# Kernel tuning notes

Hardware: AMD Instinct MI355X
Metric: run time of the kernel (lower is better)

## Reference

```python
import jax, jax.numpy as jnp
import numpy as np

N = 50000       # nodes
E = 800000      # edges (before self loops)
F_IN = 256      # num_features
HID = 64        # hidden_dim
HEADS = 4       # num_heads
NEG = 0.2       # negative_slope
LN_EPS = 1e-5


def setup_inputs() -> dict:
    key = jax.random.key(0)
    ks = jax.random.split(key, 24)
    g = lambda k, shape, s=0.05: jax.random.normal(k, shape, jnp.float32) * s
    inp = {
        "x": jax.random.normal(ks[0], (N, F_IN), jnp.float32),
        "edge_index": jax.random.randint(ks[1], (2, E), 0, N, jnp.int32),
        # gat1: in=F_IN, out=HID per head, HEADS heads, concat=True
        "W1": g(ks[2], (HEADS * HID, F_IN)),
        "att_src1": g(ks[3], (HEADS, HID)),
        "att_dst1": g(ks[4], (HEADS, HID)),
        "b1": g(ks[5], (HEADS * HID,)),
        # gat2: in=HEADS*HID, out=HID, 1 head
        "W2": g(ks[6], (HID, HEADS * HID)),
        "att_src2": g(ks[7], (1, HID)),
        "att_dst2": g(ks[8], (1, HID)),
        "b2": g(ks[9], (HID,)),
        # lin_in residual projection
        "lin_w": g(ks[10], (HID, F_IN)),
        "lin_b": g(ks[11], (HID,)),
        # LayerNorm
        "gamma": jnp.ones((HID,), jnp.float32),
        "beta": jnp.zeros((HID,), jnp.float32),
        # GRU (1 layer, input=HID, hidden=HID), gate order r,z,n as in torch
        "w_ih": g(ks[12], (3 * HID, HID)),
        "w_hh": g(ks[13], (3 * HID, HID)),
        "b_ih": g(ks[14], (3 * HID,)),
        "b_hh": g(ks[15], (3 * HID,)),
        # fc head -> 3 classes
        "fc_w": g(ks[16], (3, HID)),
        "fc_b": g(ks[17], (3,)),
    }
    return inp


def gat_conv(x, W, att_src, att_dst, bias, src, dst, heads, n_nodes):
    """PyG-style GATConv (eval mode: no dropout). src/dst include self loops."""
    h = (x @ W.T).reshape(n_nodes, heads, -1)            # [N,H,C]
    a_src = jnp.einsum('nhc,hc->nh', h, att_src)          # [N,H]
    a_dst = jnp.einsum('nhc,hc->nh', h, att_dst)
    e = jax.nn.leaky_relu(a_src[src] + a_dst[dst], NEG)   # [E',H]
    m = jax.ops.segment_max(e, dst, num_segments=n_nodes) # scatter-softmax over dst
    e = jnp.exp(e - m[dst])
    s = jax.ops.segment_sum(e, dst, num_segments=n_nodes)
    alpha = e / s[dst]                                    # [E',H]
    out = jax.ops.segment_sum(alpha[:, :, None] * h[src], dst, num_segments=n_nodes)
    return out.reshape(n_nodes, -1) + bias                # concat heads + bias


def reference(x, edge_index, W1, att_src1, att_dst1, b1, W2, att_src2, att_dst2, b2,
              lin_w, lin_b, gamma, beta, w_ih, w_hh, b_ih, b_hh, fc_w, fc_b):
    n = x.shape[0]
    loops = jnp.arange(n, dtype=edge_index.dtype)
    src = jnp.concatenate([edge_index[0], loops])  # add_self_loops=True default
    dst = jnp.concatenate([edge_index[1], loops])

    h = jax.nn.leaky_relu(gat_conv(x, W1, att_src1, att_dst1, b1, src, dst, HEADS, n), NEG)
    # F.dropout is identity in eval mode
    h = gat_conv(h, W2, att_src2, att_dst2, b2, src, dst, 1, n)
    h = jax.nn.leaky_relu(h, NEG)
    # LayerNorm (torch uses biased variance)
    mu = h.mean(-1, keepdims=True)
    var = ((h - mu) ** 2).mean(-1, keepdims=True)
    h = (h - mu) / jnp.sqrt(var + LN_EPS) * gamma + beta
    h = h + x @ lin_w.T + lin_b
    # single-step GRU with h0 = 0 (seq_len == 1)
    gi = h @ w_ih.T + b_ih                 # [N,3C]
    i_r, i_z, i_n = jnp.split(gi, 3, axis=-1)
    h_r, h_z, h_n = jnp.split(b_hh, 3)     # W_hh @ 0 == 0
    r = jax.nn.sigmoid(i_r + h_r)
    z = jax.nn.sigmoid(i_z + h_z)
    ng = jnp.tanh(i_n + r * h_n)
    hy = (1.0 - z) * ng                    # + z * h_prev(=0)
    return hy @ fc_w.T + fc_b              # [N,3]
```

## Files before the change

kernel.cpp:

```cpp
#include <hip/hip_runtime.h>
#include <hip/hip_bf16.h>

#define N_NODES 50000
#define N_EDGES 800000
#define F_IN 256
#define HID 64
#define HEADS 4
#define NEG 0.2f
#define LN_EPS 1e-5f

typedef _Float16 half8 __attribute__((ext_vector_type(8)));
typedef _Float16 half4v __attribute__((ext_vector_type(4)));
typedef _Float16 half2v __attribute__((ext_vector_type(2)));
typedef float floatx4 __attribute__((ext_vector_type(4)));

union H2U { unsigned u; half2v h; };
union H8U { half8 v; half2v h2[4]; };

__device__ __forceinline__ float wave_sum(float v) {
    #pragma unroll
    for (int o = 32; o > 0; o >>= 1) v += __shfl_xor(v, o, 64);
    return v;
}
__device__ __forceinline__ float leaky(float x) { return x > 0.0f ? x : NEG * x; }

__global__ void bucket_scatter(const int* __restrict__ src, const int* __restrict__ dst,
                               int* __restrict__ deg, int* __restrict__ colb,
                               int E, int Etot) {
    int e = blockIdx.x * blockDim.x + threadIdx.x;
    if (e >= Etot) return;
    int s, d;
    if (e < E) { s = src[e]; d = dst[e]; }
    else       { s = d = e - E; }
    int pos = atomicAdd(&deg[d], 1);
    if (pos < 64) colb[d * 64 + pos] = s;
}

struct CvtJob { const float* src; _Float16* dst; int len; };
__global__ void cvt_f16_multi(CvtJob j0, CvtJob j1, CvtJob j2, CvtJob j3, CvtJob j4) {
    int idx = (blockIdx.x * blockDim.x + threadIdx.x) * 4;
    const float* s; _Float16* d; int rel = idx;
    if      (rel < j0.len) { s = j0.src; d = j0.dst; }
    else if ((rel -= j0.len) < j1.len) { s = j1.src; d = j1.dst; }
    else if ((rel -= j1.len) < j2.len) { s = j2.src; d = j2.dst; }
    else if ((rel -= j2.len) < j3.len) { s = j3.src; d = j3.dst; }
    else if ((rel -= j3.len) < j4.len) { s = j4.src; d = j4.dst; }
    else return;
    float4 v = *(const float4*)(s + rel);
    half4v h;
    h[0] = (_Float16)v.x; h[1] = (_Float16)v.y;
    h[2] = (_Float16)v.z; h[3] = (_Float16)v.w;
    *(half4v*)(d + rel) = h;
}

__device__ __forceinline__ half8 load_a8(const _Float16* p) { return *(const half8*)p; }
__device__ __forceinline__ half8 load_a8(const float* p) {
    float4 f0 = *(const float4*)p;
    float4 f1 = *(const float4*)(p + 4);
    half8 h;
    h[0] = (_Float16)f0.x; h[1] = (_Float16)f0.y;
    h[2] = (_Float16)f0.z; h[3] = (_Float16)f0.w;
    h[4] = (_Float16)f1.x; h[5] = (_Float16)f1.y;
    h[6] = (_Float16)f1.z; h[7] = (_Float16)f1.w;
    return h;
}

template<int NT, int H, typename OutT, typename AT>
__global__ __launch_bounds__(256, 2)
void gemm_mfma(const AT* __restrict__ A, const _Float16* __restrict__ B,
               const float* __restrict__ bias, OutT* __restrict__ Cout,
               const float* __restrict__ att_s, const float* __restrict__ att_d,
               float* __restrict__ a_srcO, float* __restrict__ a_dstO,
               int M, int K, int bias_mode) {
    constexpr int Nc = NT * 16;
    constexpr int BROW = 40;
    constexpr int BTILE = Nc * BROW * 2;
    constexpr int TILEB = 16 * Nc * sizeof(OutT);
    constexpr int SM = (BTILE > 4 * TILEB) ? BTILE : 4 * TILEB;
    __shared__ __align__(16) char smem[SM];
    _Float16* sB = (_Float16*)smem;
    int tid = threadIdx.x;
    int w = tid >> 6, lane = tid & 63;
    int m_base = blockIdx.x * 64 + w * 16;
    bool active = (m_base < M);
    int r = lane & 15, q = lane >> 4;
    const AT* ap = A + (size_t)(m_base + r) * K + q * 8;
    floatx4 acc[NT];
    #pragma unroll
    for (int t = 0; t < NT; ++t) acc[t] = (floatx4){0.f, 0.f, 0.f, 0.f};
    half8 a_next = {};
    if (active) a_next = load_a8(ap);
    for (int k0 = 0; k0 < K; k0 += 32) {
        for (int i = tid; i < Nc * 4; i += 256) {
            int row = i >> 2, seg = i & 3;
            *(half8*)(sB + row * BROW + seg * 8) =
                *(const half8*)(B + (size_t)row * K + k0 + seg * 8);
        }
        __syncthreads();
        half8 a = a_next;
        if (active && k0 + 32 < K) a_next = load_a8(ap + k0 + 32);
        if (active) {
            half8 b[NT];
            #pragma unroll
            for (int t = 0; t < NT; ++t)
                b[t] = *(const half8*)(sB + (t * 16 + r) * BROW + q * 8);
            #pragma unroll
            for (int t = 0; t < NT; ++t)
                acc[t] = __builtin_amdgcn_mfma_f32_16x16x32_f16(a, b[t], acc[t], 0, 0, 0);
        }
        __syncthreads();
    }
    if (active) {
        OutT* st = (OutT*)(smem + w * TILEB);
        #pragma unroll
        for (int t = 0; t < NT; ++t) {
            int cc = t * 16 + r;
            float bv = 0.f;
            if (bias_mode == 1) bv = bias[cc];
            else if (bias_mode == 2 && cc >= 256) bv = bias[cc - 256];
            #pragma unroll
            for (int rr = 0; rr < 4; ++rr)
                st[(q * 4 + rr) * Nc + cc] = (OutT)(acc[t][rr] + bv);
        }
        constexpr int NISS = TILEB / 1024;
        const int4* src = (const int4*)st;
        int4* dst = (int4*)((char*)Cout + (size_t)m_base * (Nc * sizeof(OutT)));
        #pragma unroll
        for (int i = 0; i < NISS; ++i) dst[i * 64 + lane] = src[i * 64 + lane];
        if constexpr (H > 0) {
            float ps[H][4], pd[H][4];
            #pragma unroll
            for (int h = 0; h < H; ++h) {
                #pragma unroll
                for (int rr = 0; rr < 4; ++rr) { ps[h][rr] = 0.f; pd[h][rr] = 0.f; }
                #pragma unroll
                for (int tt = 0; tt < 4; ++tt) {
                    int t = h * 4 + tt;
                    float as = att_s[t * 16 + r];
                    float ad = att_d[t * 16 + r];
                    #pragma unroll
                    for (int rr = 0; rr < 4; ++rr) {
                        ps[h][rr] += acc[t][rr] * as;
                        pd[h][rr] += acc[t][rr] * ad;
                    }
                }
            }
            #pragma unroll
            for (int m = 1; m < 16; m <<= 1) {
                #pragma unroll
                for (int h = 0; h < H; ++h)
                    #pragma unroll
                    for (int rr = 0; rr < 4; ++rr) {
                        ps[h][rr] += __shfl_xor(ps[h][rr], m, 64);
                        pd[h][rr] += __shfl_xor(pd[h][rr], m, 64);
                    }
            }
            if (r == 0) {
                #pragma unroll
                for (int rr = 0; rr < 4; ++rr) {
                    int gm = m_base + q * 4 + rr;
                    #pragma unroll
                    for (int h = 0; h < H; ++h) {
                        a_srcO[gm * H + h] = ps[h][rr];
                        a_dstO[gm * H + h] = pd[h][rr];
                    }
                }
            }
        }
    }
}

__global__ void gat_agg4(const _Float16* __restrict__ h, const float* __restrict__ a_src,
                         const float* __restrict__ a_dst, const int* __restrict__ degA,
                         const int* __restrict__ colb, const float* __restrict__ bias,
                         _Float16* __restrict__ outp, int N) {
    int w = threadIdx.x >> 6, lane = threadIdx.x & 63;
    int i = blockIdx.x * 4 + w;
    if (i >= N) return;
    __shared__ unsigned alphS[4][256];
    __shared__ int      scolS[4][64];
    unsigned* alph = alphS[w];
    int*      scol = scolS[w];
    int deg = degA[i];
    deg = deg > 64 ? 64 : deg;
    float4 ad4 = *(const float4*)(a_dst + i * 4);

    float e0 = 0.f, e1 = 0.f, e2 = 0.f, e3 = 0.f; int s = 0;
    if (lane < deg) {
        s = colb[i * 64 + lane];
        float4 as4 = *(const float4*)(a_src + (size_t)s * 4);
        e0 = __expf(leaky(as4.x + ad4.x));
        e1 = __expf(leaky(as4.y + ad4.y));
        e2 = __expf(leaky(as4.z + ad4.z));
        e3 = __expf(leaky(as4.w + ad4.w));
    }
    float s0 = wave_sum(e0), s1 = wave_sum(e1), s2 = wave_sum(e2), s3 = wave_sum(e3);
    float4 al = make_float4(0.f, 0.f, 0.f, 0.f);
    int so = 0;
    if (lane < deg) {
        al = make_float4(e0 / s0, e1 / s1, e2 / s2, e3 / s3);
        so = s * 640;
    }
    H2U p0, p1, p2, p3;
    _Float16 t0 = (_Float16)al.x; p0.h = (half2v){t0, t0};
    _Float16 t1 = (_Float16)al.y; p1.h = (half2v){t1, t1};
    _Float16 t2 = (_Float16)al.z; p2.h = (half2v){t2, t2};
    _Float16 t3 = (_Float16)al.w; p3.h = (half2v){t3, t3};
    *(uint4*)(alph + lane * 4) = make_uint4(p0.u, p1.u, p2.u, p3.u);
    scol[lane] = so;
    int half32 = lane >> 5;
    int fl = lane & 31;
    int flb = fl * 16;
    int ahofs = half32 * 4 + (fl >> 3);
    const char* hB = (const char*)h;
    float acc[8];
    #pragma unroll
    for (int k = 0; k < 8; ++k) acc[k] = 0.f;
    int dpad = (deg + 7) & ~7;
    for (int j = 0; j < dpad; j += 8) {
        int o0 = scol[j + half32];
        int o1 = scol[j + 2 + half32];
        int o2 = scol[j + 4 + half32];
        int o3 = scol[j + 6 + half32];
        H8U v0, v1, v2, v3;
        v0.v = *(const half8*)(hB + (flb + o0));
        v1.v = *(const half8*)(hB + (flb + o1));
        v2.v = *(const half8*)(hB + (flb + o2));
        v3.v = *(const half8*)(hB + (flb + o3));
        H2U a0, a1, a2, a3;
        a0.u = alph[j * 4 + ahofs];
        a1.u = alph[j * 4 + 8 + ahofs];
        a2.u = alph[j * 4 + 16 + ahofs];
        a3.u = alph[j * 4 + 24 + ahofs];
        #pragma unroll
        for (int p = 0; p < 4; ++p) {
            half2v hp = a0.h * v0.h2[p];
            hp = __builtin_elementwise_fma(a1.h, v1.h2[p], hp);
            hp = __builtin_elementwise_fma(a2.h, v2.h2[p], hp);
            hp = __builtin_elementwise_fma(a3.h, v3.h2[p], hp);
            acc[p * 2]     += (float)hp[0];
            acc[p * 2 + 1] += (float)hp[1];
        }
    }
    #pragma unroll
    for (int k = 0; k < 8; ++k) acc[k] += __shfl_xor(acc[k], 32, 64);
    if (lane < 32) {
        half8 o8;
        #pragma unroll
        for (int k = 0; k < 8; ++k)
            o8[k] = (_Float16)leaky(acc[k] + bias[fl * 8 + k]);
        *(half8*)(outp + (size_t)i * 256 + fl * 8) = o8;
    }
}

__global__ void gat_agg1_ln(const _Float16* __restrict__ h, const float* __restrict__ a_src,
                            const float* __restrict__ a_dst, const int* __restrict__ degA,
                            const int* __restrict__ colb, const float* __restrict__ bias,
                            const _Float16* __restrict__ linh, const float* __restrict__ gamma,
                            const float* __restrict__ beta, _Float16* __restrict__ hresh,
                            int N) {
    int w = threadIdx.x >> 6, lane = threadIdx.x & 63;
    int i = blockIdx.x * 4 + w;
    if (i >= N) return;
    __shared__ unsigned alphS[4][80];
    __shared__ int      scolS[4][80];
    unsigned* alph = alphS[w];
    int*      scol = scolS[w];
    int deg = degA[i];
    deg = deg > 64 ? 64 : deg;
    float ad = a_dst[i];
    int f0 = (lane & 7) * 8;
    float acc[8];
    #pragma unroll
    for (int k = 0; k < 8; ++k) acc[k] = 0.f;

    float e = 0.f; int s = 0;
    if (lane < deg) {
        s = colb[i * 64 + lane];
        e = __expf(leaky(a_src[s] + ad));
    }
    float ss = wave_sum(e);
    H2U pa; pa.u = 0;
    int so = 0;
    if (lane < deg) {
        _Float16 ah = (_Float16)(e / ss);
        pa.h = (half2v){ah, ah};
        so = s << 7;
    }
    alph[lane] = pa.u;
    scol[lane] = so;
    if (lane < 16) { alph[64 + lane] = 0; scol[64 + lane] = 0; }
    int g = lane >> 3;
    int fb = (lane & 7) * 16;
    const char* hB = (const char*)h;
    int dpad = (deg + 15) & ~15;
    for (int j = 0; j < dpad; j += 16) {
        int o0 = scol[j + g];
        int o1 = scol[j + 8 + g];
        H8U v0, v1;
        v0.v = *(const half8*)(hB + (fb + o0));
        v1.v = *(const half8*)(hB + (fb + o1));
        H2U a0, a1;
        a0.u = alph[j + g];
        a1.u = alph[j + 8 + g];
        #pragma unroll
        for (int p = 0; p < 4; ++p) {
            half2v hp = a0.h * v0.h2[p];
            hp = __builtin_elementwise_fma(a1.h, v1.h2[p], hp);
            acc[p * 2]     += (float)hp[0];
            acc[p * 2 + 1] += (float)hp[1];
        }
    }
    #pragma unroll
    for (int k = 0; k < 8; ++k) {
        acc[k] += __shfl_xor(acc[k], 8, 64);
        acc[k] += __shfl_xor(acc[k], 16, 64);
        acc[k] += __shfl_xor(acc[k], 32, 64);
    }
    float4 b0 = *(const float4*)(bias + f0);
    float4 b1 = *(const float4*)(bias + f0 + 4);
    float o[8];
    o[0] = leaky(acc[0] + b0.x); o[1] = leaky(acc[1] + b0.y);
    o[2] = leaky(acc[2] + b0.z); o[3] = leaky(acc[3] + b0.w);
    o[4] = leaky(acc[4] + b1.x); o[5] = leaky(acc[5] + b1.y);
    o[6] = leaky(acc[6] + b1.z); o[7] = leaky(acc[7] + b1.w);
    float ls = 0.f;
    #pragma unroll
    for (int k = 0; k < 8; ++k) ls += o[k];
    ls += __shfl_xor(ls, 1, 64); ls += __shfl_xor(ls, 2, 64); ls += __shfl_xor(ls, 4, 64);
    float mu = ls * (1.0f / 64.0f);
    float lq = 0.f;
    #pragma unroll
    for (int k = 0; k < 8; ++k) { o[k] -= mu; lq += o[k] * o[k]; }
    lq += __shfl_xor(lq, 1, 64); lq += __shfl_xor(lq, 2, 64); lq += __shfl_xor(lq, 4, 64);
    float rstd = rsqrtf(lq * (1.0f / 64.0f) + LN_EPS);
    float4 g0 = *(const float4*)(gamma + f0);
    float4 g1 = *(const float4*)(gamma + f0 + 4);
    float4 be0 = *(const float4*)(beta + f0);
    float4 be1 = *(const float4*)(beta + f0 + 4);
    half8 l8 = *(const half8*)(linh + (size_t)i * 320 + f0);
    if (lane < 8) {
        half8 hv;
        hv[0] = (_Float16)(o[0] * rstd * g0.x + be0.x + (float)l8[0]);
        hv[1] = (_Float16)(o[1] * rstd * g0.y + be0.y + (float)l8[1]);
        hv[2] = (_Float16)(o[2] * rstd * g0.z + be0.z + (float)l8[2]);
        hv[3] = (_Float16)(o[3] * rstd * g0.w + be0.w + (float)l8[3]);
        hv[4] = (_Float16)(o[4] * rstd * g1.x + be1.x + (float)l8[4]);
        hv[5] = (_Float16)(o[5] * rstd * g1.y + be1.y + (float)l8[5]);
        hv[6] = (_Float16)(o[6] * rstd * g1.z + be1.z + (float)l8[6]);
        hv[7] = (_Float16)(o[7] * rstd * g1.w + be1.w + (float)l8[7]);
        *(half8*)(hresh + (size_t)i * 64 + f0) = hv;
    }
}

__global__ __launch_bounds__(256, 2)
void gemm_gru(const _Float16* __restrict__ A, const _Float16* __restrict__ B,
              const float* __restrict__ b_ih, const float* __restrict__ b_hh,
              const float* __restrict__ fc_w, const float* __restrict__ fc_b,
              float* __restrict__ outp, int M) {
    const int K = 64, NT = 12, Nc = 192;
    constexpr int BROW = 40;
    __shared__ __align__(16) char smem[4 * 16 * 192 * 2];
    _Float16* sB = (_Float16*)smem;
    int tid = threadIdx.x;
    int w = tid >> 6, lane = tid & 63;
    int m_base = blockIdx.x * 64 + w * 16;
    bool active = (m_base < M);
    int r = lane & 15, q = lane >> 4;
    const _Float16* ap = A + (size_t)(m_base + r) * K + q * 8;
    floatx4 acc[NT];
    #pragma unroll
    for (int t = 0; t < NT; ++t) acc[t] = (floatx4){0.f, 0.f, 0.f, 0.f};
    half8 a_next = {};
    if (active) a_next = *(const half8*)ap;
    for (int k0 = 0; k0 < K; k0 += 32) {
        for (int i = tid; i < Nc * 4; i += 256) {
            int row = i >> 2, seg = i & 3;
            *(half8*)(sB + row * BROW + seg * 8) =
                *(const half8*)(B + (size_t)row * K + k0 + seg * 8);
        }
        __syncthreads();
        half8 a = a_next;
        if (active && k0 + 32 < K) a_next = *(const half8*)(ap + k0 + 32);
        if (active) {
            half8 b[NT];
            #pragma unroll
            for (int t = 0; t < NT; ++t)
                b[t] = *(const half8*)(sB + (t * 16 + r) * BROW + q * 8);
            #pragma unroll
            for (int t = 0; t < NT; ++t)
                acc[t] = __builtin_amdgcn_mfma_f32_16x16x32_f16(a, b[t], acc[t], 0, 0, 0);
        }
        __syncthreads();
    }
    if (!active) return;
    _Float16* sw = (_Float16*)smem + w * 16 * 192;
    #pragma unroll
    for (int t = 0; t < NT; ++t) {
        int cc = t * 16 + r;
        float bv = b_ih[cc];
        #pragma unroll
        for (int rr = 0; rr < 4; ++rr)
            sw[(q * 4 + rr) * Nc + cc] = (_Float16)(acc[t][rr] + bv);
    }
    float br_[4], bz_[4], bn_[4], f0_[4], f1_[4], f2_[4];
    *(float4*)br_ = *(const float4*)(b_hh + r * 4);
    *(float4*)bz_ = *(const float4*)(b_hh + 64 + r * 4);
    *(float4*)bn_ = *(const float4*)(b_hh + 128 + r * 4);
    *(float4*)f0_ = *(const float4*)(fc_w + r * 4);
    *(float4*)f1_ = *(const float4*)(fc_w + 64 + r * 4);
    *(float4*)f2_ = *(const float4*)(fc_w + 128 + r * 4);
    #pragma unroll
    for (int rr = 0; rr < 4; ++rr) {
        int row = q * 4 + rr;
        const _Float16* g = sw + row * Nc;
        half4v ir4 = *(const half4v*)(g + r * 4);
        half4v iz4 = *(const half4v*)(g + 64 + r * 4);
        half4v in4 = *(const half4v*)(g + 128 + r * 4);
        float p0 = 0.f, p1 = 0.f, p2 = 0.f;
        #pragma unroll
        for (int k = 0; k < 4; ++k) {
            float rg = 1.0f / (1.0f + __expf(-((float)ir4[k] + br_[k])));
            float zg = 1.0f / (1.0f + __expf(-((float)iz4[k] + bz_[k])));
            float ng = tanhf((float)in4[k] + rg * bn_[k]);
            float hy = (1.0f - zg) * ng;
            p0 += hy * f0_[k]; p1 += hy * f1_[k]; p2 += hy * f2_[k];
        }
        #pragma unroll
        for (int o = 1; o <= 8; o <<= 1) {
            p0 += __shfl_xor(p0, o, 64);
            p1 += __shfl_xor(p1, o, 64);
            p2 += __shfl_xor(p2, o, 64);
        }
        if (r == 0) {
            int gm = m_base + row;
            outp[(size_t)gm * 3 + 0] = p0 + fc_b[0];
            outp[(size_t)gm * 3 + 1] = p1 + fc_b[1];
            outp[(size_t)gm * 3 + 2] = p2 + fc_b[2];
        }
    }
}

extern "C" void kernel_launch(void* const* d_in, const int* in_sizes, int n_in,
                              void* d_out, int out_size, void* d_ws, size_t ws_size,
                              hipStream_t stream) {
    const float* x        = (const float*)d_in[0];
    const int*   ei       = (const int*)d_in[1];
    const float* W1       = (const float*)d_in[2];
    const float* att_src1 = (const float*)d_in[3];
    const float* att_dst1 = (const float*)d_in[4];
    const float* b1       = (const float*)d_in[5];
    const float* W2       = (const float*)d_in[6];
    const float* att_src2 = (const float*)d_in[7];
    const float* att_dst2 = (const float*)d_in[8];
    const float* b2       = (const float*)d_in[9];
    const float* lin_w    = (const float*)d_in[10];
    const float* lin_b    = (const float*)d_in[11];
    const float* gamma    = (const float*)d_in[12];
    const float* beta     = (const float*)d_in[13];
    const float* w_ih     = (const float*)d_in[14];
    const float* b_ih     = (const float*)d_in[16];
    const float* b_hh     = (const float*)d_in[17];
    const float* fc_w     = (const float*)d_in[18];
    const float* fc_b     = (const float*)d_in[19];
    float* out = (float*)d_out;

    const int N = N_NODES, E = N_EDGES;
    const int Etot = E + N;
    char* ws = (char*)d_ws;

    size_t off = 0;
    auto alloc = [&](size_t bytes) {
        size_t o = off;
        off = (off + bytes + 255) & ~(size_t)255;
        return o;
    };
    int*      deg     = (int*)(ws + alloc((size_t)N * 4));
    int*      colb    = (int*)(ws + alloc((size_t)N * 64 * 4));
    float*    a_src1b = (float*)(ws + alloc((size_t)N * HEADS * 4));
    float*    a_dst1b = (float*)(ws + alloc((size_t)N * HEADS * 4));
    float*    a_src2b = (float*)(ws + alloc((size_t)N * 4));
    float*    a_dst2b = (float*)(ws + alloc((size_t)N * 4));
    _Float16* B1big   = (_Float16*)(ws + alloc((size_t)320 * 256 * 2));
    _Float16* W1h     = B1big;
    _Float16* lin_wh  = B1big + 256 * 256;
    _Float16* W2h     = (_Float16*)(ws + alloc((size_t)64 * 256 * 2));
    _Float16* w_ihh   = (_Float16*)(ws + alloc((size_t)192 * 64 * 2));
    _Float16* h1L  = (_Float16*)(ws + alloc((size_t)32000000));
    char* r3 = ws + alloc((size_t)25600000);
    _Float16* o1h   = (_Float16*)r3;
    _Float16* hresh = (_Float16*)r3;
    char* r4 = ws + alloc((size_t)6400000);
    _Float16* h2h = (_Float16*)r4;

    hipMemsetAsync(deg, 0, (size_t)N * 4, stream);

    bucket_scatter<<<(Etot + 255) / 256, 256, 0, stream>>>(ei, ei + E, deg, colb, E, Etot);

    {
        CvtJob j0{W1, W1h, 256 * 256};
        CvtJob j1{W2, W2h, 64 * 256};
        CvtJob j2{lin_w, lin_wh, 64 * 256};
        CvtJob j3{w_ih, w_ihh, 192 * 64};
        CvtJob j4{nullptr, nullptr, 0};
        int total4 = (j0.len + j1.len + j2.len + j3.len) / 4;
        cvt_f16_multi<<<(total4 + 255) / 256, 256, 0, stream>>>(j0, j1, j2, j3, j4);
    }

    const int gmBlocks = (N + 63) / 64;
    const int aggBlocks = (N + 3) / 4;

    gemm_mfma<20, 4, _Float16, float><<<gmBlocks, 256, 0, stream>>>(x, B1big, lin_b, h1L,
        att_src1, att_dst1, a_src1b, a_dst1b, N, 256, 2);
    gat_agg4<<<aggBlocks, 256, 0, stream>>>(h1L, a_src1b, a_dst1b, deg, colb, b1, o1h, N);

    gemm_mfma<4, 1, _Float16, _Float16><<<gmBlocks, 256, 0, stream>>>(o1h, W2h, nullptr, h2h,
        att_src2, att_dst2, a_src2b, a_dst2b, N, 256, 0);

    gat_agg1_ln<<<aggBlocks, 256, 0, stream>>>(h2h, a_src2b, a_dst2b, deg, colb, b2,
        h1L + 256, gamma, beta, hresh, N);

    gemm_gru<<<gmBlocks, 256, 0, stream>>>(hresh, w_ihh, b_ih, b_hh, fc_w, fc_b, out, N);
}
```

Before: 322.8 us.

## Fuse W2 projection into layer-1 aggregation and GRU head into layer-2 aggregation

The W2 GEMM with its attention dot products moves into gat_agg4 as a per-wave fdot2 matvec over an LDS row, so the 256-wide o1 intermediate no longer round-trips through global memory. The GRU input GEMM and FC head move into gat_agg1_ln the same way, which removes the separate gemm_gru kernel and the hresh buffer. Edge bucketing and weight conversion merge into one prep kernel, and W2 and w_ih are pre-transposed into k-pair-major layouts for coalesced per-lane loads. The cost is that MFMA tensor-core GEMMs become scalar dot2 matvecs that reread weights per node, which could make the aggregation kernels compute- or cache-bound.

```diff
diff --git a/kernel.cpp b/kernel.cpp
--- a/kernel.cpp
+++ b/kernel.cpp
@@ -24,33 +24,60 @@
 }
 __device__ __forceinline__ float leaky(float x) { return x > 0.0f ? x : NEG * x; }
 
-__global__ void bucket_scatter(const int* __restrict__ src, const int* __restrict__ dst,
-                               int* __restrict__ deg, int* __restrict__ colb,
-                               int E, int Etot) {
-    int e = blockIdx.x * blockDim.x + threadIdx.x;
-    if (e >= Etot) return;
-    int s, d;
-    if (e < E) { s = src[e]; d = dst[e]; }
-    else       { s = d = e - E; }
-    int pos = atomicAdd(&deg[d], 1);
-    if (pos < 64) colb[d * 64 + pos] = s;
-}
-
-struct CvtJob { const float* src; _Float16* dst; int len; };
-__global__ void cvt_f16_multi(CvtJob j0, CvtJob j1, CvtJob j2, CvtJob j3, CvtJob j4) {
-    int idx = (blockIdx.x * blockDim.x + threadIdx.x) * 4;
-    const float* s; _Float16* d; int rel = idx;
-    if      (rel < j0.len) { s = j0.src; d = j0.dst; }
-    else if ((rel -= j0.len) < j1.len) { s = j1.src; d = j1.dst; }
-    else if ((rel -= j1.len) < j2.len) { s = j2.src; d = j2.dst; }
-    else if ((rel -= j2.len) < j3.len) { s = j3.src; d = j3.dst; }
-    else if ((rel -= j3.len) < j4.len) { s = j4.src; d = j4.dst; }
-    else return;
-    float4 v = *(const float4*)(s + rel);
-    half4v h;
-    h[0] = (_Float16)v.x; h[1] = (_Float16)v.y;
-    h[2] = (_Float16)v.z; h[3] = (_Float16)v.w;
-    *(half4v*)(d + rel) = h;
+__device__ __forceinline__ float dot2acc(half2v a, half2v b, float c) {
+#if __has_builtin(__builtin_amdgcn_fdot2)
+    return __builtin_amdgcn_fdot2(a, b, c, false);
+#else
+    half2v p = a * b;
+    return c + (float)p[0] + (float)p[1];
+#endif
+}
+
+__global__ void prep_kernel(const int* __restrict__ src, const int* __restrict__ dst,
+                            int* __restrict__ deg, int* __restrict__ colb,
+                            const float* __restrict__ W1, const float* __restrict__ lin_w,
+                            _Float16* __restrict__ B1big,
+                            const float* __restrict__ W2, _Float16* __restrict__ w2p,
+                            const float* __restrict__ w_ih, _Float16* __restrict__ wihp,
+                            int E, int Etot, int SB) {
+    if ((int)blockIdx.x < SB) {
+        int e = blockIdx.x * 256 + threadIdx.x;
+        if (e >= Etot) return;
+        int s, d;
+        if (e < E) { s = src[e]; d = dst[e]; }
+        else       { s = d = e - E; }
+        int pos = atomicAdd(&deg[d], 1);
+        if (pos < 64) colb[d * 64 + pos] = s;
+        return;
+    }
+    int t = (blockIdx.x - SB) * 256 + threadIdx.x;
+    if (t < 20480) {
+        int rel = t * 4;
+        const float* s; _Float16* d;
+        if (rel < 65536) { s = W1; d = B1big; }
+        else { rel -= 65536; s = lin_w; d = B1big + 65536; }
+        float4 v = *(const float4*)(s + rel);
+        half4v h;
+        h[0] = (_Float16)v.x; h[1] = (_Float16)v.y;
+        h[2] = (_Float16)v.z; h[3] = (_Float16)v.w;
+        *(half4v*)(d + rel) = h;
+    } else {
+        int t2 = t - 20480;
+        if (t2 < 8192) {
+            int c = t2 & 63, k2 = t2 >> 6;
+            half2v h;
+            h[0] = (_Float16)W2[c * 256 + 2 * k2];
+            h[1] = (_Float16)W2[c * 256 + 2 * k2 + 1];
+            *(half2v*)(w2p + (k2 * 64 + c) * 2) = h;
+        } else if (t2 < 8192 + 6144) {
+            int t3 = t2 - 8192;
+            int c = t3 % 192, k2 = t3 / 192;
+            half2v h;
+            h[0] = (_Float16)w_ih[c * 64 + 2 * k2];
+            h[1] = (_Float16)w_ih[c * 64 + 2 * k2 + 1];
+            *(half2v*)(wihp + (k2 * 192 + c) * 2) = h;
+        }
+    }
 }
 
 __device__ __forceinline__ half8 load_a8(const _Float16* p) { return *(const half8*)p; }
@@ -173,14 +200,19 @@
 __global__ void gat_agg4(const _Float16* __restrict__ h, const float* __restrict__ a_src,
                          const float* __restrict__ a_dst, const int* __restrict__ degA,
                          const int* __restrict__ colb, const float* __restrict__ bias,
-                         _Float16* __restrict__ outp, int N) {
+                         const _Float16* __restrict__ w2p,
+                         const float* __restrict__ att_s2, const float* __restrict__ att_d2,
+                         _Float16* __restrict__ h2h, float* __restrict__ a_src2,
+                         float* __restrict__ a_dst2, int N) {
     int w = threadIdx.x >> 6, lane = threadIdx.x & 63;
     int i = blockIdx.x * 4 + w;
     if (i >= N) return;
     __shared__ unsigned alphS[4][256];
     __shared__ int      scolS[4][64];
+    __shared__ __align__(16) _Float16 o1rowS[4][256];
     unsigned* alph = alphS[w];
     int*      scol = scolS[w];
+    _Float16* o1row = o1rowS[w];
     int deg = degA[i];
     deg = deg > 64 ? 64 : deg;
     float4 ad4 = *(const float4*)(a_dst + i * 4);
@@ -249,23 +281,47 @@
         #pragma unroll
         for (int k = 0; k < 8; ++k)
             o8[k] = (_Float16)leaky(acc[k] + bias[fl * 8 + k]);
-        *(half8*)(outp + (size_t)i * 256 + fl * 8) = o8;
-    }
+        *(half8*)(o1row + fl * 8) = o8;
+    }
+    const unsigned* o1u = (const unsigned*)o1row;
+    const unsigned* w2c = (const unsigned*)w2p + lane;
+    float h2a = 0.f, h2b = 0.f;
+    #pragma unroll 4
+    for (int k2 = 0; k2 < 128; k2 += 2) {
+        H2U ov0, ov1, wv0, wv1;
+        ov0.u = o1u[k2];
+        ov1.u = o1u[k2 + 1];
+        wv0.u = w2c[k2 * 64];
+        wv1.u = w2c[(k2 + 1) * 64];
+        h2a = dot2acc(ov0.h, wv0.h, h2a);
+        h2b = dot2acc(ov1.h, wv1.h, h2b);
+    }
+    float h2c = h2a + h2b;
+    h2h[(size_t)i * 64 + lane] = (_Float16)h2c;
+    float ps = h2c * att_s2[lane];
+    float pd = h2c * att_d2[lane];
+    ps = wave_sum(ps); pd = wave_sum(pd);
+    if (lane == 0) { a_src2[i] = ps; a_dst2[i] = pd; }
 }
 
 __global__ void gat_agg1_ln(const _Float16* __restrict__ h, const float* __restrict__ a_src,
                             const float* __restrict__ a_dst, const int* __restrict__ degA,
                             const int* __restrict__ colb, const float* __restrict__ bias,
                             const _Float16* __restrict__ linh, const float* __restrict__ gamma,
-                            const float* __restrict__ beta, _Float16* __restrict__ hresh,
+                            const float* __restrict__ beta,
+                            const _Float16* __restrict__ wihp, const float* __restrict__ b_ih,
+                            const float* __restrict__ b_hh, const float* __restrict__ fc_w,
+                            const float* __restrict__ fc_b, float* __restrict__ outp,
                             int N) {
     int w = threadIdx.x >> 6, lane = threadIdx.x & 63;
     int i = blockIdx.x * 4 + w;
     if (i >= N) return;
     __shared__ unsigned alphS[4][80];
     __shared__ int      scolS[4][80];
+    __shared__ __align__(16) _Float16 hrowS[4][64];
     unsigned* alph = alphS[w];
     int*      scol = scolS[w];
+    _Float16* hrow = hrowS[w];
     int deg = degA[i];
     deg = deg > 64 ? 64 : deg;
     float ad = a_dst[i];
@@ -334,12 +390,12 @@
     for (int k = 0; k < 8; ++k) { o[k] -= mu; lq += o[k] * o[k]; }
     lq += __shfl_xor(lq, 1, 64); lq += __shfl_xor(lq, 2, 64); lq += __shfl_xor(lq, 4, 64);
     float rstd = rsqrtf(lq * (1.0f / 64.0f) + LN_EPS);
-    float4 g0 = *(const float4*)(gamma + f0);
-    float4 g1 = *(const float4*)(gamma + f0 + 4);
-    float4 be0 = *(const float4*)(beta + f0);
-    float4 be1 = *(const float4*)(beta + f0 + 4);
-    half8 l8 = *(const half8*)(linh + (size_t)i * 320 + f0);
     if (lane < 8) {
+        float4 g0 = *(const float4*)(gamma + f0);
+        float4 g1 = *(const float4*)(gamma + f0 + 4);
+        float4 be0 = *(const float4*)(beta + f0);
+        float4 be1 = *(const float4*)(beta + f0 + 4);
+        half8 l8 = *(const half8*)(linh + (size_t)i * 320 + f0);
         half8 hv;
         hv[0] = (_Float16)(o[0] * rstd * g0.x + be0.x + (float)l8[0]);
         hv[1] = (_Float16)(o[1] * rstd * g0.y + be0.y + (float)l8[1]);
@@ -349,95 +405,36 @@
         hv[5] = (_Float16)(o[5] * rstd * g1.y + be1.y + (float)l8[5]);
         hv[6] = (_Float16)(o[6] * rstd * g1.z + be1.z + (float)l8[6]);
         hv[7] = (_Float16)(o[7] * rstd * g1.w + be1.w + (float)l8[7]);
-        *(half8*)(hresh + (size_t)i * 64 + f0) = hv;
-    }
-}
-
-__global__ __launch_bounds__(256, 2)
-void gemm_gru(const _Float16* __restrict__ A, const _Float16* __restrict__ B,
-              const float* __restrict__ b_ih, const float* __restrict__ b_hh,
-              const float* __restrict__ fc_w, const float* __restrict__ fc_b,
-              float* __restrict__ outp, int M) {
-    const int K = 64, NT = 12, Nc = 192;
-    constexpr int BROW = 40;
-    __shared__ __align__(16) char smem[4 * 16 * 192 * 2];
-    _Float16* sB = (_Float16*)smem;
-    int tid = threadIdx.x;
-    int w = tid >> 6, lane = tid & 63;
-    int m_base = blockIdx.x * 64 + w * 16;
-    bool active = (m_base < M);
-    int r = lane & 15, q = lane >> 4;
-    const _Float16* ap = A + (size_t)(m_base + r) * K + q * 8;
-    floatx4 acc[NT];
-    #pragma unroll
-    for (int t = 0; t < NT; ++t) acc[t] = (floatx4){0.f, 0.f, 0.f, 0.f};
-    half8 a_next = {};
-    if (active) a_next = *(const half8*)ap;
-    for (int k0 = 0; k0 < K; k0 += 32) {
-        for (int i = tid; i < Nc * 4; i += 256) {
-            int row = i >> 2, seg = i & 3;
-            *(half8*)(sB + row * BROW + seg * 8) =
-                *(const half8*)(B + (size_t)row * K + k0 + seg * 8);
-        }
-        __syncthreads();
-        half8 a = a_next;
-        if (active && k0 + 32 < K) a_next = *(const half8*)(ap + k0 + 32);
-        if (active) {
-            half8 b[NT];
-            #pragma unroll
-            for (int t = 0; t < NT; ++t)
-                b[t] = *(const half8*)(sB + (t * 16 + r) * BROW + q * 8);
-            #pragma unroll
-            for (int t = 0; t < NT; ++t)
-                acc[t] = __builtin_amdgcn_mfma_f32_16x16x32_f16(a, b[t], acc[t], 0, 0, 0);
-        }
-        __syncthreads();
-    }
-    if (!active) return;
-    _Float16* sw = (_Float16*)smem + w * 16 * 192;
-    #pragma unroll
-    for (int t = 0; t < NT; ++t) {
-        int cc = t * 16 + r;
-        float bv = b_ih[cc];
-        #pragma unroll
-        for (int rr = 0; rr < 4; ++rr)
-            sw[(q * 4 + rr) * Nc + cc] = (_Float16)(acc[t][rr] + bv);
-    }
-    float br_[4], bz_[4], bn_[4], f0_[4], f1_[4], f2_[4];
-    *(float4*)br_ = *(const float4*)(b_hh + r * 4);
-    *(float4*)bz_ = *(const float4*)(b_hh + 64 + r * 4);
-    *(float4*)bn_ = *(const float4*)(b_hh + 128 + r * 4);
-    *(float4*)f0_ = *(const float4*)(fc_w + r * 4);
-    *(float4*)f1_ = *(const float4*)(fc_w + 64 + r * 4);
-    *(float4*)f2_ = *(const float4*)(fc_w + 128 + r * 4);
-    #pragma unroll
-    for (int rr = 0; rr < 4; ++rr) {
-        int row = q * 4 + rr;
-        const _Float16* g = sw + row * Nc;
-        half4v ir4 = *(const half4v*)(g + r * 4);
-        half4v iz4 = *(const half4v*)(g + 64 + r * 4);
-        half4v in4 = *(const half4v*)(g + 128 + r * 4);
-        float p0 = 0.f, p1 = 0.f, p2 = 0.f;
-        #pragma unroll
-        for (int k = 0; k < 4; ++k) {
-            float rg = 1.0f / (1.0f + __expf(-((float)ir4[k] + br_[k])));
-            float zg = 1.0f / (1.0f + __expf(-((float)iz4[k] + bz_[k])));
-            float ng = tanhf((float)in4[k] + rg * bn_[k]);
-            float hy = (1.0f - zg) * ng;
-            p0 += hy * f0_[k]; p1 += hy * f1_[k]; p2 += hy * f2_[k];
-        }
-        #pragma unroll
-        for (int o = 1; o <= 8; o <<= 1) {
-            p0 += __shfl_xor(p0, o, 64);
-            p1 += __shfl_xor(p1, o, 64);
-            p2 += __shfl_xor(p2, o, 64);
-        }
-        if (r == 0) {
-            int gm = m_base + row;
-            outp[(size_t)gm * 3 + 0] = p0 + fc_b[0];
-            outp[(size_t)gm * 3 + 1] = p1 + fc_b[1];
-            outp[(size_t)gm * 3 + 2] = p2 + fc_b[2];
-        }
+        *(half8*)(hrow + f0) = hv;
+    }
+    const unsigned* hu = (const unsigned*)hrow;
+    const unsigned* wr = (const unsigned*)wihp + lane;
+    const unsigned* wz = (const unsigned*)wihp + 64 + lane;
+    const unsigned* wn = (const unsigned*)wihp + 128 + lane;
+    float gr = b_ih[lane], gz = b_ih[64 + lane], gn = b_ih[128 + lane];
+    #pragma unroll 4
+    for (int k2 = 0; k2 < 32; ++k2) {
+        H2U hv2, w0, w1, w2v;
+        hv2.u = hu[k2];
+        w0.u = wr[k2 * 192];
+        w1.u = wz[k2 * 192];
+        w2v.u = wn[k2 * 192];
+        gr = dot2acc(hv2.h, w0.h, gr);
+        gz = dot2acc(hv2.h, w1.h, gz);
+        gn = dot2acc(hv2.h, w2v.h, gn);
+    }
+    float rg = 1.0f / (1.0f + __expf(-(gr + b_hh[lane])));
+    float zg = 1.0f / (1.0f + __expf(-(gz + b_hh[64 + lane])));
+    float ng = tanhf(gn + rg * b_hh[128 + lane]);
+    float hy = (1.0f - zg) * ng;
+    float q0 = hy * fc_w[lane];
+    float q1 = hy * fc_w[64 + lane];
+    float q2 = hy * fc_w[128 + lane];
+    q0 = wave_sum(q0); q1 = wave_sum(q1); q2 = wave_sum(q2);
+    if (lane == 0) {
+        outp[(size_t)i * 3 + 0] = q0 + fc_b[0];
+        outp[(size_t)i * 3 + 1] = q1 + fc_b[1];
+        outp[(size_t)i * 3 + 2] = q2 + fc_b[2];
     }
 }
 
@@ -482,43 +479,27 @@
     float*    a_src2b = (float*)(ws + alloc((size_t)N * 4));
     float*    a_dst2b = (float*)(ws + alloc((size_t)N * 4));
     _Float16* B1big   = (_Float16*)(ws + alloc((size_t)320 * 256 * 2));
-    _Float16* W1h     = B1big;
-    _Float16* lin_wh  = B1big + 256 * 256;
-    _Float16* W2h     = (_Float16*)(ws + alloc((size_t)64 * 256 * 2));
-    _Float16* w_ihh   = (_Float16*)(ws + alloc((size_t)192 * 64 * 2));
+    _Float16* w2p     = (_Float16*)(ws + alloc((size_t)64 * 256 * 2));
+    _Float16* wihp    = (_Float16*)(ws + alloc((size_t)192 * 64 * 2));
     _Float16* h1L  = (_Float16*)(ws + alloc((size_t)32000000));
-    char* r3 = ws + alloc((size_t)25600000);
-    _Float16* o1h   = (_Float16*)r3;
-    _Float16* hresh = (_Float16*)r3;
-    char* r4 = ws + alloc((size_t)6400000);
-    _Float16* h2h = (_Float16*)r4;
+    _Float16* h2h  = (_Float16*)(ws + alloc((size_t)6400000));
 
     hipMemsetAsync(deg, 0, (size_t)N * 4, stream);
 
-    bucket_scatter<<<(Etot + 255) / 256, 256, 0, stream>>>(ei, ei + E, deg, colb, E, Etot);
-
-    {
-        CvtJob j0{W1, W1h, 256 * 256};
-        CvtJob j1{W2, W2h, 64 * 256};
-        CvtJob j2{lin_w, lin_wh, 64 * 256};
-        CvtJob j3{w_ih, w_ihh, 192 * 64};
-        CvtJob j4{nullptr, nullptr, 0};
-        int total4 = (j0.len + j1.len + j2.len + j3.len) / 4;
-        cvt_f16_multi<<<(total4 + 255) / 256, 256, 0, stream>>>(j0, j1, j2, j3, j4);
-    }
+    const int SB = (Etot + 255) / 256;
+    const int CB = (20480 + 8192 + 6144 + 255) / 256;
+    prep_kernel<<<SB + CB, 256, 0, stream>>>(ei, ei + E, deg, colb,
+        W1, lin_w, B1big, W2, w2p, w_ih, wihp, E, Etot, SB);
 
     const int gmBlocks = (N + 63) / 64;
     const int aggBlocks = (N + 3) / 4;
 
     gemm_mfma<20, 4, _Float16, float><<<gmBlocks, 256, 0, stream>>>(x, B1big, lin_b, h1L,
         att_src1, att_dst1, a_src1b, a_dst1b, N, 256, 2);
-    gat_agg4<<<aggBlocks, 256, 0, stream>>>(h1L, a_src1b, a_dst1b, deg, colb, b1, o1h, N);
-
-    gemm_mfma<4, 1, _Float16, _Float16><<<gmBlocks, 256, 0, stream>>>(o1h, W2h, nullptr, h2h,
-        att_src2, att_dst2, a_src2b, a_dst2b, N, 256, 0);
+
+    gat_agg4<<<aggBlocks, 256, 0, stream>>>(h1L, a_src1b, a_dst1b, deg, colb, b1,
+        w2p, att_src2, att_dst2, h2h, a_src2b, a_dst2b, N);
 
     gat_agg1_ln<<<aggBlocks, 256, 0, stream>>>(h2h, a_src2b, a_dst2b, deg, colb, b2,
-        h1L + 256, gamma, beta, hresh, N);
-
-    gemm_gru<<<gmBlocks, 256, 0, stream>>>(hresh, w_ihh, b_ih, b_hh, fc_w, fc_b, out, N);
-}
+        h1L + 256, gamma, beta, wihp, b_ih, b_hh, fc_w, fc_b, out, N);
+}
```

Result: slower. 358.7 us (+11.1%).
